# Kernel optimization log

Hardware: AMD Instinct MI355X
Metric: run time of the kernel (lower is better)

The kernel has to match this reference:

```python
import jax, jax.numpy as jnp
import numpy as np


def _pairwise_sqdist(x, y):
    # x: [B, N, 3], y: [B, M, 3] -> [B, N, M] squared distances
    x2 = jnp.sum(x * x, axis=-1, keepdims=True)          # [B, N, 1]
    y2 = jnp.sum(y * y, axis=-1)[:, None, :]             # [B, 1, M]
    xy = jnp.einsum('bnd,bmd->bnm', x, y)                # [B, N, M]
    return jnp.maximum(x2 + y2 - 2.0 * xy, 0.0)


def _chamfer_l1(x, y):
    # PoinTr-style ChamferDistanceL1: mean sqrt NN dist both ways, averaged
    d = _pairwise_sqdist(x, y)                           # [B, N, M]
    d1 = jnp.sqrt(jnp.min(d, axis=2))                    # x -> nearest in y
    d2 = jnp.sqrt(jnp.min(d, axis=1))                    # y -> nearest in x
    return 0.5 * (jnp.mean(d1) + jnp.mean(d2))


def setup_inputs() -> dict:
    key = jax.random.key(0)
    k1, k2, k3, k4 = jax.random.split(key, 4)
    B, Nc, Nf = 4, 1024, 8192
    return {
        'ret_coarse': jax.random.normal(k1, (B, Nc, 3), dtype=jnp.float32),
        'ret_fine':   jax.random.normal(k2, (B, Nf, 3), dtype=jnp.float32),
        'gt_fine':    jax.random.normal(k3, (B, Nf, 3), dtype=jnp.float32),
        'gt_coarse':  jax.random.normal(k4, (B, Nc, 3), dtype=jnp.float32),
    }


def reference(ret_coarse, ret_fine, gt_fine, gt_coarse):
    loss_fine = _chamfer_l1(ret_fine, gt_fine)
    # coarse L2 point-distance loss: mean over (B, Nc) of per-point L2 norm
    loss_coarse = jnp.mean(jnp.sqrt(jnp.sum((ret_coarse - gt_coarse) ** 2, axis=2)))
    return (loss_coarse, loss_fine)
```

## Files before the change

kernel.cpp:

```cpp
#include <hip/hip_runtime.h>

#define B  4
#define NF 8192
#define NC 1024
#define TJ (NF / 32)
#define TPW (TJ / 8)
#define XT 128

#define NCRS (B * NC)

typedef _Float16 h8   __attribute__((ext_vector_type(8)));
typedef float    f16v __attribute__((ext_vector_type(16)));


__global__ __launch_bounds__(256) void k_prep(const float* __restrict__ rf,
                                              const float* __restrict__ gf,
                                              h8* __restrict__ fragbuf,
                                              const float* __restrict__ rc,
                                              const float* __restrict__ gc,
                                              float* __restrict__ out) {
    int id  = blockIdx.x * 256 + threadIdx.x;
    int src = id >> 16;
    int rem = id & 65535;
    int b   = rem >> 14;
    int jt  = (rem >> 6) & (TJ - 1);
    int ln  = rem & 63;
    int n   = ln & 31, kg = ln >> 5;

    const float* y = (src ? rf : gf) + ((size_t)(b * NF) + jt * 32 + n) * 3;
    float y0 = y[0], y1 = y[1], y2 = y[2];
    _Float16 h0 = (_Float16)y0, h1 = (_Float16)y1, h2 = (_Float16)y2;
    _Float16 l0 = (_Float16)(y0 - (float)h0);
    _Float16 l1 = (_Float16)(y1 - (float)h1);
    _Float16 l2 = (_Float16)(y2 - (float)h2);
    float sy = fmaf(y0, y0, fmaf(y1, y1, y2 * y2));
    _Float16 sh = (_Float16)sy;
    _Float16 sl = (_Float16)(sy - (float)sh);

    h8 fr = {};
    if (kg == 0) {
        fr[0] = h0; fr[1] = h1; fr[2] = h2;
        fr[3] = l0; fr[4] = l1; fr[5] = l2;
        fr[6] = h0; fr[7] = h1;
    } else {
        fr[0] = h2; fr[1] = sh; fr[2] = sl;
        fr[3] = (_Float16)1.0f; fr[4] = (_Float16)1.0f;
    }
    fragbuf[((size_t)(src * B + b) * TJ + jt) * 64 + ln] = fr;

    if (id < NCRS) {
        float dx = rc[3 * id + 0] - gc[3 * id + 0];
        float dy = rc[3 * id + 1] - gc[3 * id + 1];
        float dz = rc[3 * id + 2] - gc[3 * id + 2];
        float s = sqrtf(fmaf(dx, dx, fmaf(dy, dy, dz * dz)));
#pragma unroll
        for (int off = 32; off > 0; off >>= 1) s += __shfl_down(s, off);
        if ((threadIdx.x & 63) == 0)
            atomicAdd(&out[0], s * (1.0f / (float)NCRS));
    }
}

__global__ __launch_bounds__(512) void k_main(const float* __restrict__ rf,
                                              const float* __restrict__ gf,
                                              const h8* __restrict__ fragbuf,
                                              float* __restrict__ out) {
    __shared__ float rbuf[8][XT];

    int bx  = blockIdx.x;
    int reg = bx & 7;
    int dir = reg >> 2;
    int b   = reg & 3;
    int xg  = bx >> 3;
    int t   = threadIdx.x;
    int ln = t & 63, w = t >> 6, m = ln & 31, kg = ln >> 5;

    const float* xp = dir ? gf : rf;
    h8 bfr[4];
#pragma unroll
    for (int f = 0; f < 4; ++f) {
        const float* xr = xp + ((size_t)(b * NF) + xg * XT + f * 32 + m) * 3;
        float x0 = xr[0], x1 = xr[1], x2 = xr[2];
        float t0 = -2.0f * x0, t1 = -2.0f * x1, t2 = -2.0f * x2;
        _Float16 mh0 = (_Float16)t0, mh1 = (_Float16)t1, mh2 = (_Float16)t2;
        _Float16 ml0 = (_Float16)(t0 - (float)mh0);
        _Float16 ml1 = (_Float16)(t1 - (float)mh1);
        _Float16 ml2 = (_Float16)(t2 - (float)mh2);
        float sx = fmaf(x0, x0, fmaf(x1, x1, x2 * x2));
        _Float16 sh = (_Float16)sx;
        _Float16 sl = (_Float16)(sx - (float)sh);
        h8 fr = {};
        if (kg == 0) {
            fr[0] = mh0; fr[1] = mh1; fr[2] = mh2;
            fr[3] = mh0; fr[4] = mh1; fr[5] = mh2;
            fr[6] = ml0; fr[7] = ml1;
        } else {
            fr[0] = ml2; fr[1] = (_Float16)1.0f; fr[2] = (_Float16)1.0f;
            fr[3] = sh;  fr[4] = sl;
        }
        bfr[f] = fr;
    }

    float mn[4];
#pragma unroll
    for (int f = 0; f < 4; ++f) mn[f] = 3.4e38f;

    const h8* p = fragbuf + ((size_t)(dir * B + b) * TJ + w * TPW) * 64 + ln;
    h8 a0 = p[0];
    h8 a1 = p[64];
#pragma unroll 2
    for (int q = 0; q < TPW / 2; ++q) {
        h8 n0 = p[(2 * q + 2) * 64];
        h8 n1 = p[(2 * q + 3) * 64];
#pragma unroll
        for (int f = 0; f < 4; ++f) {
            f16v c0 = __builtin_amdgcn_mfma_f32_32x32x16_f16(a0, bfr[f], (f16v){}, 0, 0, 0);
            f16v c1 = __builtin_amdgcn_mfma_f32_32x32x16_f16(a1, bfr[f], (f16v){}, 0, 0, 0);
            float pa = fminf(c0[0], c1[0]);
            float pb = fminf(c0[1], c1[1]);
#pragma unroll
            for (int r = 2; r < 16; r += 2) {
                pa = fminf(fminf(c0[r], c1[r]), pa);
                pb = fminf(fminf(c0[r + 1], c1[r + 1]), pb);
            }
            mn[f] = fminf(fminf(pa, pb), mn[f]);
        }
        a0 = n0;
        a1 = n1;
    }

#pragma unroll
    for (int f = 0; f < 4; ++f) {
        float v = fminf(mn[f], __shfl_xor(mn[f], 32));
        if (kg == 0) rbuf[w][f * 32 + m] = v;
    }
    __syncthreads();
    if (t < XT) {
        float v = rbuf[0][t];
#pragma unroll
        for (int ww = 1; ww < 8; ++ww) v = fminf(v, rbuf[ww][t]);
        float s = sqrtf(fmaxf(v, 0.0f));
#pragma unroll
        for (int off = 32; off > 0; off >>= 1) s += __shfl_down(s, off);
        if ((t & 63) == 0)
            atomicAdd(&out[1], s * (0.5f / (float)(B * NF)));
    }
}

extern "C" void kernel_launch(void* const* d_in, const int* in_sizes, int n_in,
                              void* d_out, int out_size, void* d_ws, size_t ws_size,
                              hipStream_t stream) {
    const float* rc = (const float*)d_in[0];
    const float* rf = (const float*)d_in[1];
    const float* gf = (const float*)d_in[2];
    const float* gc = (const float*)d_in[3];

    h8*    fragbuf = (h8*)d_ws;
    float* out     = (float*)d_out;

    hipMemsetAsync(out, 0, 2 * sizeof(float), stream);
    k_prep<<<512, 256, 0, stream>>>(rf, gf, fragbuf, rc, gc, out);
    k_main<<<512, 512, 0, stream>>>(rf, gf, fragbuf, out);
}
```

Before: 87.13 us.

## Fuse prep and main into one cooperative kernel with grid sync, larger x tile

Merges the fragment-prep kernel, the memset and the chamfer main kernel into a single cooperative launch separated by a grid-wide sync. The output is zeroed in-kernel and atomics are reduced to one per block. The x tile per block doubles to 256, halving the grid to 256 blocks, and each wave holds 8 B-fragments, so A-fragment loads are reused across more columns. The aims are to remove launch and memset overhead and to cut fragbuf traffic, at the cost of more registers, fewer blocks, and a grid-sync barrier. The in-kernel zeroing of out[1] is not ordered against atomics from other blocks except through the grid sync, which does come first, so it is safe.

```diff
diff --git a/kernel.cpp b/kernel.cpp
--- a/kernel.cpp
+++ b/kernel.cpp
@@ -1,83 +1,84 @@
 #include <hip/hip_runtime.h>
+#include <hip/hip_cooperative_groups.h>
 
 #define B  4
 #define NF 8192
 #define NC 1024
 #define TJ (NF / 32)
 #define TPW (TJ / 8)
-#define XT 128
+#define XT 256
 
 #define NCRS (B * NC)
 
 typedef _Float16 h8   __attribute__((ext_vector_type(8)));
 typedef float    f16v __attribute__((ext_vector_type(16)));
 
+namespace cg = cooperative_groups;
 
-__global__ __launch_bounds__(256) void k_prep(const float* __restrict__ rf,
-                                              const float* __restrict__ gf,
-                                              h8* __restrict__ fragbuf,
-                                              const float* __restrict__ rc,
-                                              const float* __restrict__ gc,
-                                              float* __restrict__ out) {
-    int id  = blockIdx.x * 256 + threadIdx.x;
-    int src = id >> 16;
-    int rem = id & 65535;
-    int b   = rem >> 14;
-    int jt  = (rem >> 6) & (TJ - 1);
-    int ln  = rem & 63;
-    int n   = ln & 31, kg = ln >> 5;
 
-    const float* y = (src ? rf : gf) + ((size_t)(b * NF) + jt * 32 + n) * 3;
-    float y0 = y[0], y1 = y[1], y2 = y[2];
-    _Float16 h0 = (_Float16)y0, h1 = (_Float16)y1, h2 = (_Float16)y2;
-    _Float16 l0 = (_Float16)(y0 - (float)h0);
-    _Float16 l1 = (_Float16)(y1 - (float)h1);
-    _Float16 l2 = (_Float16)(y2 - (float)h2);
-    float sy = fmaf(y0, y0, fmaf(y1, y1, y2 * y2));
-    _Float16 sh = (_Float16)sy;
-    _Float16 sl = (_Float16)(sy - (float)sh);
+__global__ __launch_bounds__(512) void k_fused(const float* __restrict__ rf,
+                                               const float* __restrict__ gf,
+                                               const float* __restrict__ rc,
+                                               const float* __restrict__ gc,
+                                               h8* __restrict__ fragbuf,
+                                               float* __restrict__ out) {
+    __shared__ float rbuf[8][XT];
+    __shared__ float crs[8];
+    __shared__ float fsum[4];
 
-    h8 fr = {};
-    if (kg == 0) {
-        fr[0] = h0; fr[1] = h1; fr[2] = h2;
-        fr[3] = l0; fr[4] = l1; fr[5] = l2;
-        fr[6] = h0; fr[7] = h1;
-    } else {
-        fr[0] = h2; fr[1] = sh; fr[2] = sl;
-        fr[3] = (_Float16)1.0f; fr[4] = (_Float16)1.0f;
+    int bx = blockIdx.x;
+    int t  = threadIdx.x;
+    int ln = t & 63, w = t >> 6, m = ln & 31, kg = ln >> 5;
+
+    {
+        int id  = bx * 512 + t;
+        int src = id >> 16;
+        int pb  = (id >> 14) & 3;
+        int jt  = (id >> 6) & (TJ - 1);
+
+        const float* y = (src ? rf : gf) + ((size_t)(pb * NF) + jt * 32 + m) * 3;
+        float y0 = y[0], y1 = y[1], y2 = y[2];
+        _Float16 h0 = (_Float16)y0, h1 = (_Float16)y1, h2 = (_Float16)y2;
+        _Float16 l0 = (_Float16)(y0 - (float)h0);
+        _Float16 l1 = (_Float16)(y1 - (float)h1);
+        _Float16 l2 = (_Float16)(y2 - (float)h2);
+        float sy = fmaf(y0, y0, fmaf(y1, y1, y2 * y2));
+        _Float16 sh = (_Float16)sy;
+        _Float16 sl = (_Float16)(sy - (float)sh);
+
+        h8 fr = {};
+        if (kg == 0) {
+            fr[0] = h0; fr[1] = h1; fr[2] = h2;
+            fr[3] = l0; fr[4] = l1; fr[5] = l2;
+            fr[6] = h0; fr[7] = h1;
+        } else {
+            fr[0] = h2; fr[1] = sh; fr[2] = sl;
+            fr[3] = (_Float16)1.0f; fr[4] = (_Float16)1.0f;
+        }
+        fragbuf[((size_t)(src * B + pb) * TJ + jt) * 64 + ln] = fr;
+
+        if (bx < 8) {
+            float dx = rc[3 * id + 0] - gc[3 * id + 0];
+            float dy = rc[3 * id + 1] - gc[3 * id + 1];
+            float dz = rc[3 * id + 2] - gc[3 * id + 2];
+            float s = sqrtf(fmaf(dx, dx, fmaf(dy, dy, dz * dz)));
+#pragma unroll
+            for (int off = 32; off > 0; off >>= 1) s += __shfl_down(s, off);
+            if (ln == 0) crs[w] = s;
+        }
+        if (bx == 0 && t == 0) { out[0] = 0.0f; out[1] = 0.0f; }
     }
-    fragbuf[((size_t)(src * B + b) * TJ + jt) * 64 + ln] = fr;
+    cg::this_grid().sync();
 
-    if (id < NCRS) {
-        float dx = rc[3 * id + 0] - gc[3 * id + 0];
-        float dy = rc[3 * id + 1] - gc[3 * id + 1];
-        float dz = rc[3 * id + 2] - gc[3 * id + 2];
-        float s = sqrtf(fmaf(dx, dx, fmaf(dy, dy, dz * dz)));
-#pragma unroll
-        for (int off = 32; off > 0; off >>= 1) s += __shfl_down(s, off);
-        if ((threadIdx.x & 63) == 0)
-            atomicAdd(&out[0], s * (1.0f / (float)NCRS));
-    }
-}
-
-__global__ __launch_bounds__(512) void k_main(const float* __restrict__ rf,
-                                              const float* __restrict__ gf,
-                                              const h8* __restrict__ fragbuf,
-                                              float* __restrict__ out) {
-    __shared__ float rbuf[8][XT];
-
-    int bx  = blockIdx.x;
     int reg = bx & 7;
     int dir = reg >> 2;
     int b   = reg & 3;
     int xg  = bx >> 3;
-    int t   = threadIdx.x;
-    int ln = t & 63, w = t >> 6, m = ln & 31, kg = ln >> 5;
 
     const float* xp = dir ? gf : rf;
-    h8 bfr[4];
+    h8 bfr[8];
 #pragma unroll
-    for (int f = 0; f < 4; ++f) {
+    for (int f = 0; f < 8; ++f) {
         const float* xr = xp + ((size_t)(b * NF) + xg * XT + f * 32 + m) * 3;
         float x0 = xr[0], x1 = xr[1], x2 = xr[2];
         float t0 = -2.0f * x0, t1 = -2.0f * x1, t2 = -2.0f * x2;
@@ -100,9 +101,9 @@
         bfr[f] = fr;
     }
 
-    float mn[4];
+    float mn[8];
 #pragma unroll
-    for (int f = 0; f < 4; ++f) mn[f] = 3.4e38f;
+    for (int f = 0; f < 8; ++f) mn[f] = 3.4e38f;
 
     const h8* p = fragbuf + ((size_t)(dir * B + b) * TJ + w * TPW) * 64 + ln;
     h8 a0 = p[0];
@@ -112,7 +113,7 @@
         h8 n0 = p[(2 * q + 2) * 64];
         h8 n1 = p[(2 * q + 3) * 64];
 #pragma unroll
-        for (int f = 0; f < 4; ++f) {
+        for (int f = 0; f < 8; ++f) {
             f16v c0 = __builtin_amdgcn_mfma_f32_32x32x16_f16(a0, bfr[f], (f16v){}, 0, 0, 0);
             f16v c1 = __builtin_amdgcn_mfma_f32_32x32x16_f16(a1, bfr[f], (f16v){}, 0, 0, 0);
             float pa = fminf(c0[0], c1[0]);
@@ -129,7 +130,7 @@
     }
 
 #pragma unroll
-    for (int f = 0; f < 4; ++f) {
+    for (int f = 0; f < 8; ++f) {
         float v = fminf(mn[f], __shfl_xor(mn[f], 32));
         if (kg == 0) rbuf[w][f * 32 + m] = v;
     }
@@ -141,8 +142,17 @@
         float s = sqrtf(fmaxf(v, 0.0f));
 #pragma unroll
         for (int off = 32; off > 0; off >>= 1) s += __shfl_down(s, off);
-        if ((t & 63) == 0)
-            atomicAdd(&out[1], s * (0.5f / (float)(B * NF)));
+        if (ln == 0) fsum[w] = s;
+    }
+    __syncthreads();
+    if (t == 0) {
+        float fine = fsum[0] + fsum[1] + fsum[2] + fsum[3];
+        atomicAdd(&out[1], fine * (0.5f / (float)(B * NF)));
+        if (bx < 8) {
+            float c = crs[0] + crs[1] + crs[2] + crs[3]
+                    + crs[4] + crs[5] + crs[6] + crs[7];
+            atomicAdd(&out[0], c * (1.0f / (float)NCRS));
+        }
     }
 }
 
@@ -157,7 +167,8 @@
     h8*    fragbuf = (h8*)d_ws;
     float* out     = (float*)d_out;
 
-    hipMemsetAsync(out, 0, 2 * sizeof(float), stream);
-    k_prep<<<512, 256, 0, stream>>>(rf, gf, fragbuf, rc, gc, out);
-    k_main<<<512, 512, 0, stream>>>(rf, gf, fragbuf, out);
+    void* args[] = {(void*)&rf, (void*)&gf, (void*)&rc, (void*)&gc,
+                    (void*)&fragbuf, (void*)&out};
+    hipLaunchCooperativeKernel((const void*)k_fused, dim3(256), dim3(512),
+                               args, 0, stream);
 }
```

Result: slower. 125.2 us (+43.7%).
